# Kernel tuning notes

Measured on AMD Instinct MI355X. Metric: run time of the kernel, lower is better.

Reference implementation:

```python
import jax, jax.numpy as jnp
import numpy as np

B, N, D, DEG = 16, 8192, 384, 16
K, H, STEPS = 8, 128, 3


def setup_inputs() -> dict:
    key = jax.random.key(0)
    ks = jax.random.split(key, 8)
    s_in = 1.0 / np.sqrt(2 * D)
    s_h = 1.0 / np.sqrt(H)
    return {
        "q_embs": jax.random.normal(ks[0], (B, D), jnp.float32),
        "emb": jax.random.normal(ks[1], (B, N, D), jnp.float32),
        "neighbors": jax.random.randint(ks[2], (B, N, DEG), 0, N, jnp.int32),
        "labels": jax.random.randint(ks[3], (B, N), 0, 2, jnp.int32),
        "W1": jax.random.normal(ks[4], (2 * D, H), jnp.float32) * s_in,
        "b1": jnp.zeros((H,), jnp.float32),
        "W2": jax.random.normal(ks[5], (H, K), jnp.float32) * s_h,
        "b2": jnp.zeros((K,), jnp.float32),
        "P1": jax.random.normal(ks[6], (2 * D, H), jnp.float32) * s_in,
        "pb1": jnp.zeros((H,), jnp.float32),
        "P2": jax.random.normal(ks[7], (H, 1), jnp.float32) * s_h,
        "pb2": jnp.zeros((1,), jnp.float32),
    }


def reference(q_embs, emb, neighbors, labels, W1, b1, W2, b2, P1, pb1, P2, pb2):
    b, n, d = emb.shape
    k = W2.shape[1]
    # inp = [emb | q broadcast]  -> [B, N, 2D]
    inp = jnp.concatenate([emb, jnp.broadcast_to(q_embs[:, None, :], emb.shape)], axis=-1)
    # path_net: sigmoid(MLP) -> [B, N], then +1 at support (label==1) nodes
    path = jax.nn.sigmoid(jax.nn.relu(inp @ P1 + pb1) @ P2 + pb2)[..., 0]
    path = path + labels.astype(path.dtype)
    # coin_net amplitudes scaled by (1 + path)
    amps = (jax.nn.relu(inp @ W1 + b1) @ W2 + b2) * (1.0 + path)[..., None]  # [B,N,K]
    # initial uniform state
    state = jnp.full((b, n, k), 1.0 / np.sqrt(n * k), dtype=emb.dtype)

    # sparse adjacency diffusion: out[i] = sum_{j in nbrs[i]} st[j]
    spmm = jax.vmap(lambda st, nb: st[nb].sum(axis=1))  # st [N,K], nb [N,DEG]

    for _ in range(STEPS):
        st = spmm(state * amps, neighbors)                 # [B,N,K]
        norm = jnp.linalg.norm(st.reshape(b, -1), axis=1)[:, None, None]
        state = jnp.where(norm > 0, st / norm, st)
    return jnp.abs(state).sum(axis=-1)  # [B,N]
```

## Files before the change

kernel.cpp:

```cpp
#include <hip/hip_runtime.h>
#include <cstdint>
#include <cstddef>

#define BB 16
#define NN 8192
#define DD 384
#define HH 128
#define KK 8
#define DEG 16

typedef short bf8_t __attribute__((ext_vector_type(8)));
typedef float f4_t __attribute__((ext_vector_type(4)));

__device__ __forceinline__ unsigned short f2bf(float f) {
  unsigned int u = __float_as_uint(f);
  u += 0x7FFFu + ((u >> 16) & 1u);
  return (unsigned short)(u >> 16);
}

__device__ __forceinline__ bf8_t pack8(float4 f0, float4 f1) {
  union { unsigned short us[8]; bf8_t v; } pk;
  pk.us[0] = f2bf(f0.x); pk.us[1] = f2bf(f0.y);
  pk.us[2] = f2bf(f0.z); pk.us[3] = f2bf(f0.w);
  pk.us[4] = f2bf(f1.x); pk.us[5] = f2bf(f1.y);
  pk.us[6] = f2bf(f1.z); pk.us[7] = f2bf(f1.w);
  return pk.v;
}

__global__ __launch_bounds__(256) void kprep(
    const float* __restrict__ q, const float* __restrict__ W1,
    const float* __restrict__ b1, const float* __restrict__ P1,
    const float* __restrict__ pb1,
    unsigned short* __restrict__ W1t, unsigned short* __restrict__ P1t,
    float* __restrict__ base1, float* __restrict__ baseP,
    float* __restrict__ normsq)
{
  int blk = blockIdx.x, t = threadIdx.x;
  if (blk < 32) {
    int b = blk >> 1, net = blk & 1;
    const float* W = (net ? P1 : W1) + (size_t)DD * HH;
    const float* qb = q + b * DD;
    int h = t & 127, half = t >> 7;
    int d0 = half * 192;
    float a0 = 0.f, a1 = 0.f, a2 = 0.f, a3 = 0.f;
    for (int d = d0; d < d0 + 192; d += 4) {
      a0 = fmaf(qb[d],     W[(size_t)d * HH + h],       a0);
      a1 = fmaf(qb[d + 1], W[(size_t)(d + 1) * HH + h], a1);
      a2 = fmaf(qb[d + 2], W[(size_t)(d + 2) * HH + h], a2);
      a3 = fmaf(qb[d + 3], W[(size_t)(d + 3) * HH + h], a3);
    }
    __shared__ float red[256];
    red[t] = (a0 + a1) + (a2 + a3);
    __syncthreads();
    if (t < 128) {
      float tot = red[t] + red[t + 128] + (net ? pb1[h] : b1[h]);
      (net ? baseP : base1)[b * HH + h] = tot;
    }
  } else {
    int e = (blk - 32) * 3072 + t;
    for (int it = 0; it < 12; ++it, e += 256) {
      int net = e / 49152;
      int r = e - net * 49152;
      int d = r >> 7;
      int h = r & 127;
      float v = (net ? P1 : W1)[d * HH + h];
      (net ? P1t : W1t)[h * DD + d] = f2bf(v);
    }
    if (blk == 32 && t < BB) normsq[t] = 0.f;
  }
}

__global__ __launch_bounds__(512, 2) void kgemm(
    const float* __restrict__ emb,
    const unsigned short* __restrict__ W1t, const unsigned short* __restrict__ P1t,
    const float* __restrict__ base1, const float* __restrict__ baseP,
    const float* __restrict__ W2, const float* __restrict__ b2,
    const float* __restrict__ P2, const float* __restrict__ pb2,
    float* __restrict__ rawamps, float* __restrict__ pslogit)
{
  __shared__ __align__(16) unsigned short sB[128 * 384];
  __shared__ float sW2a[128 * 9];
  __shared__ float sBase[128];
  __shared__ float sP2[128];
  __shared__ float sB2[8];

  const int g = blockIdx.x;
  const int slot = g & 7;
  const int net = (g >> 3) & 1;
  const int wid = (g >> 4) * 8 + slot;
  const int b = wid >> 5;
  const int rowbase = (wid & 31) * 256;

  const int t = threadIdx.x;
  const int w = t >> 6, lane = t & 63, q = lane >> 4, ln = lane & 15;

  const unsigned short* Wt = net ? P1t : W1t;
  {
    int h = t >> 2, p0 = t & 3;
#pragma unroll
    for (int i = 0; i < 12; ++i) {
      int p = p0 + i * 4;
      uint4 v = *(const uint4*)(Wt + h * DD + p * 8);
      *(uint4*)((char*)sB + h * 768 + ((p ^ (h & 7)) << 4)) = v;
    }
  }
  if (t < 128) sBase[t] = (net ? baseP : base1)[b * HH + t];
  if (net == 0) {
    for (int e = t; e < HH * KK; e += 512) {
      int h = e >> 3, kk = e & 7;
      sW2a[h * 9 + kk] = W2[e];
    }
    if (t < 8) sB2[t] = b2[t];
  } else if (t >= 128 && t < 256) {
    sP2[t - 128] = P2[t - 128];
  }

  const float* ar0 = emb + (size_t)(b * NN + rowbase + w * 32 + ln) * DD + q * 8;
  const float* ar1 = ar0 + (size_t)16 * DD;
  float4 pf[2][4];
  pf[0][0] = ((const float4*)ar0)[0];        pf[0][1] = ((const float4*)ar0)[1];
  pf[0][2] = ((const float4*)ar1)[0];        pf[0][3] = ((const float4*)ar1)[1];
  pf[1][0] = ((const float4*)(ar0 + 32))[0]; pf[1][1] = ((const float4*)(ar0 + 32))[1];
  pf[1][2] = ((const float4*)(ar1 + 32))[0]; pf[1][3] = ((const float4*)(ar1 + 32))[1];

  f4_t acc[2][8];
  f4_t zero = {0.f, 0.f, 0.f, 0.f};
#pragma unroll
  for (int i = 0; i < 8; ++i) { acc[0][i] = zero; acc[1][i] = zero; }

  __syncthreads();

#pragma unroll
  for (int j = 0; j < 12; ++j) {
    const int s = j & 1;
    bf8_t af0 = pack8(pf[s][0], pf[s][1]);
    bf8_t af1 = pack8(pf[s][2], pf[s][3]);
    if (j + 2 < 12) {
      const float* p0 = ar0 + (j + 2) * 32;
      const float* p1 = ar1 + (j + 2) * 32;
      pf[s][0] = ((const float4*)p0)[0]; pf[s][1] = ((const float4*)p0)[1];
      pf[s][2] = ((const float4*)p1)[0]; pf[s][3] = ((const float4*)p1)[1];
    }
    const int jb = j * 4;
#pragma unroll
    for (int ct = 0; ct < 8; ++ct) {
      const int h = ct * 16 + ln;
      bf8_t bf = *(const bf8_t*)((const char*)sB + h * 768 + (((jb + q) ^ (ln & 7)) << 4));
      acc[0][ct] = __builtin_amdgcn_mfma_f32_16x16x32_bf16(af0, bf, acc[0][ct], 0, 0, 0);
      acc[1][ct] = __builtin_amdgcn_mfma_f32_16x16x32_bf16(af1, bf, acc[1][ct], 0, 0, 0);
    }
  }

  const float pb2v = pb2[0];
#pragma unroll
  for (int grp = 0; grp < 2; ++grp) {
#pragma unroll
    for (int r = 0; r < 4; ++r) {
      const int grow = rowbase + w * 32 + grp * 16 + q * 4 + r;
      if (net == 0) {
        float s[8];
#pragma unroll
        for (int kk = 0; kk < 8; ++kk) s[kk] = 0.f;
#pragma unroll
        for (int ct = 0; ct < 8; ++ct) {
          int col = ct * 16 + ln;
          float h1 = fmaxf(acc[grp][ct][r] + sBase[col], 0.f);
#pragma unroll
          for (int kk = 0; kk < 8; ++kk) s[kk] = fmaf(h1, sW2a[col * 9 + kk], s[kk]);
        }
#pragma unroll
        for (int off = 1; off < 16; off <<= 1)
#pragma unroll
          for (int kk = 0; kk < 8; ++kk) s[kk] += __shfl_xor(s[kk], off, 64);
        if (ln == 0) {
          float4 o0, o1;
          o0.x = s[0] + sB2[0]; o0.y = s[1] + sB2[1];
          o0.z = s[2] + sB2[2]; o0.w = s[3] + sB2[3];
          o1.x = s[4] + sB2[4]; o1.y = s[5] + sB2[5];
          o1.z = s[6] + sB2[6]; o1.w = s[7] + sB2[7];
          float4* dst = (float4*)(rawamps + (size_t)(b * NN + grow) * KK);
          dst[0] = o0; dst[1] = o1;
        }
      } else {
        float ps = 0.f;
#pragma unroll
        for (int ct = 0; ct < 8; ++ct) {
          int col = ct * 16 + ln;
          float hp = fmaxf(acc[grp][ct][r] + sBase[col], 0.f);
          ps = fmaf(hp, sP2[col], ps);
        }
#pragma unroll
        for (int off = 1; off < 16; off <<= 1) ps += __shfl_xor(ps, off, 64);
        if (ln == 0) pslogit[b * NN + grow] = ps + pb2v;
      }
    }
  }
}

__global__ __launch_bounds__(256) void applyscale(
    const float* __restrict__ raw, const float* __restrict__ psl,
    const int* __restrict__ lab, float* __restrict__ ampsP)
{
  int node = blockIdx.x * 256 + threadIdx.x;
  float sc = 1.f + 1.f / (1.f + __expf(-psl[node])) + (float)lab[node];
  const float4* r = (const float4*)(raw + (size_t)node * KK);
  float4 v0 = r[0], v1 = r[1];
  float2* p = (float2*)ampsP;
  p[0 * (BB * NN) + node] = make_float2(v0.x * sc, v0.y * sc);
  p[1 * (BB * NN) + node] = make_float2(v0.z * sc, v0.w * sc);
  p[2 * (BB * NN) + node] = make_float2(v1.x * sc, v1.y * sc);
  p[3 * (BB * NN) + node] = make_float2(v1.z * sc, v1.w * sc);
}

template<bool MUL, bool NRM>
__global__ __launch_bounds__(256) void sgl(
    const int* __restrict__ nbr, const float* __restrict__ src,
    const float* __restrict__ mult, float* __restrict__ out,
    float* __restrict__ normsq)
{
  __shared__ float2 sS[NN];
  const int g = blockIdx.x;
  const int kp = g & 3;
  const int rep = (g >> 2) & 7;
  const int b = g >> 5;
  const int t = threadIdx.x;

  const size_t pb = (size_t)kp * (BB * NN) + (size_t)b * NN;
  {
    const float4* p4 = (const float4*)((const float2*)src + pb);
    float4* s4 = (float4*)sS;
#pragma unroll
    for (int i = 0; i < 16; ++i) s4[t + i * 256] = p4[t + i * 256];
  }
  __syncthreads();

  const float2* mplane = (const float2*)mult + pb;
  float2* oplane = (float2*)out + pb;
  float ssacc = 0.f;
#pragma unroll
  for (int u = 0; u < 4; ++u) {
    int n = rep * 1024 + u * 256 + t;
    const int4* nbp = (const int4*)(nbr + ((size_t)b * NN + n) * DEG);
    int4 q0 = nbp[0], q1 = nbp[1], q2 = nbp[2], q3 = nbp[3];
    float ax = 0.f, ay = 0.f;
    float2 v;
    v = sS[q0.x]; ax += v.x; ay += v.y;
    v = sS[q0.y]; ax += v.x; ay += v.y;
    v = sS[q0.z]; ax += v.x; ay += v.y;
    v = sS[q0.w]; ax += v.x; ay += v.y;
    v = sS[q1.x]; ax += v.x; ay += v.y;
    v = sS[q1.y]; ax += v.x; ay += v.y;
    v = sS[q1.z]; ax += v.x; ay += v.y;
    v = sS[q1.w]; ax += v.x; ay += v.y;
    v = sS[q2.x]; ax += v.x; ay += v.y;
    v = sS[q2.y]; ax += v.x; ay += v.y;
    v = sS[q2.z]; ax += v.x; ay += v.y;
    v = sS[q2.w]; ax += v.x; ay += v.y;
    v = sS[q3.x]; ax += v.x; ay += v.y;
    v = sS[q3.y]; ax += v.x; ay += v.y;
    v = sS[q3.z]; ax += v.x; ay += v.y;
    v = sS[q3.w]; ax += v.x; ay += v.y;
    if (MUL) { float2 m = mplane[n]; ax *= m.x; ay *= m.y; }
    oplane[n] = make_float2(ax, ay);
    if (NRM) ssacc += ax * ax + ay * ay;
  }
  if (NRM) {
#pragma unroll
    for (int o = 1; o < 64; o <<= 1) ssacc += __shfl_xor(ssacc, o, 64);
    if ((t & 63) == 0) atomicAdd(&normsq[b], ssacc);
  }
}

__global__ __launch_bounds__(256) void fout(
    const float* __restrict__ u, const float* __restrict__ normsq,
    float* __restrict__ out)
{
  int node = blockIdx.x * 256 + threadIdx.x;
  float ns = normsq[node >> 13];
  float inv = ns > 0.f ? rsqrtf(ns) : 1.f;
  const float2* p = (const float2*)u;
  float2 v0 = p[0 * (BB * NN) + node];
  float2 v1 = p[1 * (BB * NN) + node];
  float2 v2 = p[2 * (BB * NN) + node];
  float2 v3 = p[3 * (BB * NN) + node];
  out[node] = (fabsf(v0.x) + fabsf(v0.y) + fabsf(v1.x) + fabsf(v1.y) +
               fabsf(v2.x) + fabsf(v2.y) + fabsf(v3.x) + fabsf(v3.y)) * inv;
}

extern "C" void kernel_launch(void* const* d_in, const int* in_sizes, int n_in,
                              void* d_out, int out_size, void* d_ws, size_t ws_size,
                              hipStream_t stream) {
  const float* q   = (const float*)d_in[0];
  const float* emb = (const float*)d_in[1];
  const int*   nbr = (const int*)d_in[2];
  const int*   lab = (const int*)d_in[3];
  const float* W1  = (const float*)d_in[4];
  const float* b1  = (const float*)d_in[5];
  const float* W2  = (const float*)d_in[6];
  const float* b2  = (const float*)d_in[7];
  const float* P1  = (const float*)d_in[8];
  const float* pb1 = (const float*)d_in[9];
  const float* P2  = (const float*)d_in[10];
  const float* pb2 = (const float*)d_in[11];
  float* out = (float*)d_out;

  const size_t NK = (size_t)BB * NN * KK;
  float* ws     = (float*)d_ws;
  float* buf0   = ws;
  float* buf1   = buf0 + NK;
  float* buf2   = buf1 + NK;
  float* psl    = buf2 + NK;
  float* base1  = psl + (size_t)BB * NN;
  float* baseP  = base1 + BB * HH;
  float* normsq = baseP + BB * HH;
  unsigned short* W1t = (unsigned short*)(normsq + 16);
  unsigned short* P1t = W1t + (size_t)HH * DD;

  kprep<<<64, 256, 0, stream>>>(q, W1, b1, P1, pb1, W1t, P1t, base1, baseP, normsq);
  kgemm<<<1024, 512, 0, stream>>>(emb, W1t, P1t, base1, baseP, W2, b2, P2, pb2,
                                  buf0, psl);
  applyscale<<<512, 256, 0, stream>>>(buf0, psl, lab, buf1);
  sgl<true,  false><<<512, 256, 0, stream>>>(nbr, buf1, buf1, buf2, normsq);
  sgl<true,  false><<<512, 256, 0, stream>>>(nbr, buf2, buf1, buf0, normsq);
  sgl<false, true ><<<512, 256, 0, stream>>>(nbr, buf0, buf0, buf1, normsq);
  fout<<<512, 256, 0, stream>>>(buf1, normsq, out);
}
```

Measured before the change: 423.1 us.

## Stream weight tile through double-buffered LDS chunks to raise GEMM occupancy

The kernel no longer stages the full 128x384 bf16 weight matrix (96 KB) in LDS. It now streams it in four K-chunks of 96 columns through a double-buffered 2x24 KB LDS area, prefetching the next chunk into registers while the MFMA loop runs on the current one. Launch bounds go from 2 to 4 blocks per CU so the smaller LDS footprint lets more blocks run at once. The cost is three extra block barriers, global weight reads spread through the main loop, and a tighter register budget from the higher launch bound, which may cause spills.

```diff
diff --git a/kernel.cpp b/kernel.cpp
--- a/kernel.cpp
+++ b/kernel.cpp
@@ -70,7 +70,7 @@
   }
 }
 
-__global__ __launch_bounds__(512, 2) void kgemm(
+__global__ __launch_bounds__(512, 4) void kgemm(
     const float* __restrict__ emb,
     const unsigned short* __restrict__ W1t, const unsigned short* __restrict__ P1t,
     const float* __restrict__ base1, const float* __restrict__ baseP,
@@ -78,7 +78,7 @@
     const float* __restrict__ P2, const float* __restrict__ pb2,
     float* __restrict__ rawamps, float* __restrict__ pslogit)
 {
-  __shared__ __align__(16) unsigned short sB[128 * 384];
+  __shared__ __align__(16) unsigned short sB[2][128 * 96];
   __shared__ float sW2a[128 * 9];
   __shared__ float sBase[128];
   __shared__ float sP2[128];
@@ -95,13 +95,18 @@
   const int w = t >> 6, lane = t & 63, q = lane >> 4, ln = lane & 15;
 
   const unsigned short* Wt = net ? P1t : W1t;
+  const int sh = t >> 2;
+  const int sp0 = t & 3;
+  const int se = sh & 3;
+  const unsigned short* wsrc = Wt + sh * DD;
+
   {
-    int h = t >> 2, p0 = t & 3;
-#pragma unroll
-    for (int i = 0; i < 12; ++i) {
-      int p = p0 + i * 4;
-      uint4 v = *(const uint4*)(Wt + h * DD + p * 8);
-      *(uint4*)((char*)sB + h * 768 + ((p ^ (h & 7)) << 4)) = v;
+    char* dst = (char*)&sB[0][0] + sh * 192;
+#pragma unroll
+    for (int i = 0; i < 3; ++i) {
+      int p = sp0 + i * 4;
+      uint4 v = *(const uint4*)(wsrc + p * 8);
+      *(uint4*)(dst + ((p ^ se) << 4)) = v;
     }
   }
   if (t < 128) sBase[t] = (net ? baseP : base1)[b * HH + t];
@@ -131,23 +136,42 @@
   __syncthreads();
 
 #pragma unroll
-  for (int j = 0; j < 12; ++j) {
-    const int s = j & 1;
-    bf8_t af0 = pack8(pf[s][0], pf[s][1]);
-    bf8_t af1 = pack8(pf[s][2], pf[s][3]);
-    if (j + 2 < 12) {
-      const float* p0 = ar0 + (j + 2) * 32;
-      const float* p1 = ar1 + (j + 2) * 32;
-      pf[s][0] = ((const float4*)p0)[0]; pf[s][1] = ((const float4*)p0)[1];
-      pf[s][2] = ((const float4*)p1)[0]; pf[s][3] = ((const float4*)p1)[1];
-    }
-    const int jb = j * 4;
-#pragma unroll
-    for (int ct = 0; ct < 8; ++ct) {
-      const int h = ct * 16 + ln;
-      bf8_t bf = *(const bf8_t*)((const char*)sB + h * 768 + (((jb + q) ^ (ln & 7)) << 4));
-      acc[0][ct] = __builtin_amdgcn_mfma_f32_16x16x32_bf16(af0, bf, acc[0][ct], 0, 0, 0);
-      acc[1][ct] = __builtin_amdgcn_mfma_f32_16x16x32_bf16(af1, bf, acc[1][ct], 0, 0, 0);
+  for (int q4 = 0; q4 < 4; ++q4) {
+    uint4 nv0, nv1, nv2;
+    if (q4 < 3) {
+      const unsigned short* src = wsrc + (q4 + 1) * 96 + sp0 * 8;
+      nv0 = *(const uint4*)(src);
+      nv1 = *(const uint4*)(src + 32);
+      nv2 = *(const uint4*)(src + 64);
+    }
+    const char* bbase = (const char*)&sB[0][0] + (q4 & 1) * 24576;
+#pragma unroll
+    for (int jl = 0; jl < 3; ++jl) {
+      const int j = q4 * 3 + jl;
+      const int s = j & 1;
+      bf8_t af0 = pack8(pf[s][0], pf[s][1]);
+      bf8_t af1 = pack8(pf[s][2], pf[s][3]);
+      if (j + 2 < 12) {
+        const float* p0 = ar0 + (j + 2) * 32;
+        const float* p1 = ar1 + (j + 2) * 32;
+        pf[s][0] = ((const float4*)p0)[0]; pf[s][1] = ((const float4*)p0)[1];
+        pf[s][2] = ((const float4*)p1)[0]; pf[s][3] = ((const float4*)p1)[1];
+      }
+      const int cb = jl * 4 + q;
+#pragma unroll
+      for (int ct = 0; ct < 8; ++ct) {
+        const int h = ct * 16 + ln;
+        bf8_t bf = *(const bf8_t*)(bbase + h * 192 + ((cb ^ (ln & 3)) << 4));
+        acc[0][ct] = __builtin_amdgcn_mfma_f32_16x16x32_bf16(af0, bf, acc[0][ct], 0, 0, 0);
+        acc[1][ct] = __builtin_amdgcn_mfma_f32_16x16x32_bf16(af1, bf, acc[1][ct], 0, 0, 0);
+      }
+    }
+    if (q4 < 3) {
+      char* dst = (char*)&sB[0][0] + ((q4 + 1) & 1) * 24576 + sh * 192;
+      *(uint4*)(dst + ((sp0 ^ se) << 4)) = nv0;
+      *(uint4*)(dst + (((sp0 + 4) ^ se) << 4)) = nv1;
+      *(uint4*)(dst + (((sp0 + 8) ^ se) << 4)) = nv2;
+      __syncthreads();
     }
   }
 
```

Result: slower. 436.4 us (+3.1%).

## Stream weight tiles into double-buffered LDS via global_load_lds to raise occupancy

Applied to the files above, without the earlier changes.

The GEMM kernel no longer stages the full 128x384 bf16 weight matrix in LDS. It now streams four 96-wide K-chunks through a two-slot buffer, using direct global-to-LDS loads that overlap with MFMA work. The prep kernel writes the transposed weights in a chunked, pre-swizzled layout that these 16-byte copies expect. The smaller LDS footprint lets launch bounds rise from 2 to 3 blocks per CU, at the cost of three extra block barriers per tile and more register pressure.

```diff
diff --git a/kernel.cpp b/kernel.cpp
--- a/kernel.cpp
+++ b/kernel.cpp
@@ -11,6 +11,13 @@
 
 typedef short bf8_t __attribute__((ext_vector_type(8)));
 typedef float f4_t __attribute__((ext_vector_type(4)));
+
+typedef const __attribute__((address_space(1))) unsigned char* gcp_t;
+typedef __attribute__((address_space(3))) unsigned char* lcp_t;
+
+__device__ __forceinline__ void glds16(const void* g, void* l) {
+  __builtin_amdgcn_global_load_lds((gcp_t)g, (lcp_t)l, 16, 0, 0);
+}
 
 __device__ __forceinline__ unsigned short f2bf(float f) {
   unsigned int u = __float_as_uint(f);
@@ -64,13 +71,17 @@
       int d = r >> 7;
       int h = r & 127;
       float v = (net ? P1 : W1)[d * HH + h];
-      (net ? P1t : W1t)[h * DD + d] = f2bf(v);
+      int q4 = d / 96;
+      int rem = d - q4 * 96;
+      int cb = rem >> 3, wi = rem & 7;
+      int c = cb ^ ((h & 3) ^ ((h >> 2) & 3));
+      (net ? P1t : W1t)[q4 * 12288 + h * 96 + c * 8 + wi] = f2bf(v);
     }
     if (blk == 32 && t < BB) normsq[t] = 0.f;
   }
 }
 
-__global__ __launch_bounds__(512, 2) void kgemm(
+__global__ __launch_bounds__(512, 3) void kgemm(
     const float* __restrict__ emb,
     const unsigned short* __restrict__ W1t, const unsigned short* __restrict__ P1t,
     const float* __restrict__ base1, const float* __restrict__ baseP,
@@ -78,7 +89,7 @@
     const float* __restrict__ P2, const float* __restrict__ pb2,
     float* __restrict__ rawamps, float* __restrict__ pslogit)
 {
-  __shared__ __align__(16) unsigned short sB[128 * 384];
+  __shared__ __align__(16) unsigned short sB[2][128 * 96];
   __shared__ float sW2a[128 * 9];
   __shared__ float sBase[128];
   __shared__ float sP2[128];
@@ -93,16 +104,16 @@
 
   const int t = threadIdx.x;
   const int w = t >> 6, lane = t & 63, q = lane >> 4, ln = lane & 15;
-
-  const unsigned short* Wt = net ? P1t : W1t;
+  const int fl = (ln & 3) ^ (ln >> 2);
+
+  const unsigned short* Wsw = net ? P1t : W1t;
+
   {
-    int h = t >> 2, p0 = t & 3;
-#pragma unroll
-    for (int i = 0; i < 12; ++i) {
-      int p = p0 + i * 4;
-      uint4 v = *(const uint4*)(Wt + h * DD + p * 8);
-      *(uint4*)((char*)sB + h * 768 + ((p ^ (h & 7)) << 4)) = v;
-    }
+    const unsigned short* src = Wsw + w * 512 + lane * 8;
+    char* dst = (char*)&sB[0][0] + w * 1024;
+    glds16(src,        dst);
+    glds16(src + 4096, dst + 8192);
+    glds16(src + 8192, dst + 16384);
   }
   if (t < 128) sBase[t] = (net ? baseP : base1)[b * HH + t];
   if (net == 0) {
@@ -131,24 +142,37 @@
   __syncthreads();
 
 #pragma unroll
-  for (int j = 0; j < 12; ++j) {
-    const int s = j & 1;
-    bf8_t af0 = pack8(pf[s][0], pf[s][1]);
-    bf8_t af1 = pack8(pf[s][2], pf[s][3]);
-    if (j + 2 < 12) {
-      const float* p0 = ar0 + (j + 2) * 32;
-      const float* p1 = ar1 + (j + 2) * 32;
-      pf[s][0] = ((const float4*)p0)[0]; pf[s][1] = ((const float4*)p0)[1];
-      pf[s][2] = ((const float4*)p1)[0]; pf[s][3] = ((const float4*)p1)[1];
-    }
-    const int jb = j * 4;
-#pragma unroll
-    for (int ct = 0; ct < 8; ++ct) {
-      const int h = ct * 16 + ln;
-      bf8_t bf = *(const bf8_t*)((const char*)sB + h * 768 + (((jb + q) ^ (ln & 7)) << 4));
-      acc[0][ct] = __builtin_amdgcn_mfma_f32_16x16x32_bf16(af0, bf, acc[0][ct], 0, 0, 0);
-      acc[1][ct] = __builtin_amdgcn_mfma_f32_16x16x32_bf16(af1, bf, acc[1][ct], 0, 0, 0);
-    }
+  for (int q4 = 0; q4 < 4; ++q4) {
+    if (q4 < 3) {
+      const unsigned short* src = Wsw + (q4 + 1) * 12288 + w * 512 + lane * 8;
+      char* dst = (char*)&sB[0][0] + ((q4 + 1) & 1) * 24576 + w * 1024;
+      glds16(src,        dst);
+      glds16(src + 4096, dst + 8192);
+      glds16(src + 8192, dst + 16384);
+    }
+    const char* bbase = (const char*)&sB[0][0] + (q4 & 1) * 24576;
+#pragma unroll
+    for (int jl = 0; jl < 3; ++jl) {
+      const int j = q4 * 3 + jl;
+      const int s = j & 1;
+      bf8_t af0 = pack8(pf[s][0], pf[s][1]);
+      bf8_t af1 = pack8(pf[s][2], pf[s][3]);
+      if (j + 2 < 12) {
+        const float* p0 = ar0 + (j + 2) * 32;
+        const float* p1 = ar1 + (j + 2) * 32;
+        pf[s][0] = ((const float4*)p0)[0]; pf[s][1] = ((const float4*)p0)[1];
+        pf[s][2] = ((const float4*)p1)[0]; pf[s][3] = ((const float4*)p1)[1];
+      }
+      const int cb = jl * 4 + q;
+#pragma unroll
+      for (int ct = 0; ct < 8; ++ct) {
+        const int h = ct * 16 + ln;
+        bf8_t bf = *(const bf8_t*)(bbase + h * 192 + (((cb ^ fl)) << 4));
+        acc[0][ct] = __builtin_amdgcn_mfma_f32_16x16x32_bf16(af0, bf, acc[0][ct], 0, 0, 0);
+        acc[1][ct] = __builtin_amdgcn_mfma_f32_16x16x32_bf16(af1, bf, acc[1][ct], 0, 0, 0);
+      }
+    }
+    if (q4 < 3) __syncthreads();
   }
 
   const float pb2v = pb2[0];
```

Result: faster. 411.0 us (-2.9%).
